# Optimization experiments

Hardware: AMD Instinct MI355X
Metric: run time of the kernel (lower is better)

## Reference

```python
import jax, jax.numpy as jnp
import numpy as np

N = 50000        # n_nodes
E = 640000       # n_edges
D = 128          # d_model (in_dim == out_dim)
H = 8            # num_heads
DH = D // H      # head dim = 16
EPS = 1e-5


def _batchnorm(x, g, b):
    # BatchNorm1d, training-mode batch statistics (biased variance)
    mu = jnp.mean(x, axis=0)
    var = jnp.mean((x - mu) ** 2, axis=0)
    return (x - mu) * jax.lax.rsqrt(var + EPS) * g + b


def setup_inputs() -> dict:
    key = jax.random.key(0)
    ks = jax.random.split(key, 16)
    s = 0.05
    h = jax.random.normal(ks[0], (N, D), jnp.float32)
    src = jax.random.randint(ks[1], (E,), 0, N)
    # guarantee every node has >= 1 incoming edge (avoids z == 0)
    dst = jnp.concatenate([jnp.arange(N), jax.random.randint(ks[2], (E - N,), 0, N)])
    return {
        "h": h,
        "src": src,
        "dst": dst,
        "WQ": jax.random.normal(ks[3], (D, D), jnp.float32) * s,
        "WK": jax.random.normal(ks[4], (D, D), jnp.float32) * s,
        "WV": jax.random.normal(ks[5], (D, D), jnp.float32) * s,
        "WO": jax.random.normal(ks[6], (D, D), jnp.float32) * s,
        "bO": jnp.zeros((D,), jnp.float32),
        "W1": jax.random.normal(ks[7], (2 * D, D), jnp.float32) * s,
        "b1": jnp.zeros((2 * D,), jnp.float32),
        "W2": jax.random.normal(ks[8], (D, 2 * D), jnp.float32) * s,
        "b2": jnp.zeros((D,), jnp.float32),
        "bn1_g": jnp.ones((D,), jnp.float32),
        "bn1_b": jnp.zeros((D,), jnp.float32),
        "bn2_g": jnp.ones((D,), jnp.float32),
        "bn2_b": jnp.zeros((D,), jnp.float32),
    }


def reference(h, src, dst, WQ, WK, WV, WO, bO, W1, b1, W2, b2, bn1_g, bn1_b, bn2_g, bn2_b):
    n = h.shape[0]
    # projections -> [N, H, DH]
    Q = (h @ WQ.T).reshape(n, H, DH)
    K = (h @ WK.T).reshape(n, H, DH)
    V = (h @ WV.T).reshape(n, H, DH)
    # per-edge score: sum(K[src] * Q[dst]) -> [E, H]; clamp/exp (scaled_exp)
    score = jnp.sum(K[src] * Q[dst], axis=-1) / np.sqrt(DH)
    score = jnp.exp(jnp.clip(score, -5.0, 5.0))
    # scatter-sum weighted values and normalizers to destination nodes
    wV = jax.ops.segment_sum(V[src] * score[..., None], dst, num_segments=n)  # [N,H,DH]
    z = jax.ops.segment_sum(score, dst, num_segments=n)                       # [N,H]
    attn = (wV / z[..., None]).reshape(n, D)
    # O projection + residual + BN1
    h1 = _batchnorm(h + (attn @ WO.T + bO), bn1_g, bn1_b)
    # FFN + residual + BN2
    f = jax.nn.relu(h1 @ W1.T + b1) @ W2.T + b2
    return _batchnorm(h1 + f, bn2_g, bn2_b)
```

## Files before the change

### kernel.cpp

```cpp
#include <hip/hip_runtime.h>
#include <math.h>


#define ND128 16384
typedef _Float16 f16;
typedef __attribute__((ext_vector_type(8))) _Float16 h8;
typedef __attribute__((ext_vector_type(4))) _Float16 h4;
typedef __attribute__((ext_vector_type(2))) _Float16 h2;
typedef __attribute__((ext_vector_type(4))) float f4;
typedef __attribute__((ext_vector_type(2))) float ff2;

__device__ __forceinline__ ff2 fp8x2_dec(unsigned v) {
#if __has_builtin(__builtin_amdgcn_cvt_pk_f32_fp8)
    return __builtin_amdgcn_cvt_pk_f32_fp8((int)v, false);
#else
    ff2 r;
    unsigned b0 = v & 0xffu, b1 = (v >> 8) & 0xffu;
    {
        unsigned e = (b0 >> 3) & 15u, m = b0 & 7u;
        float x = e ? __uint_as_float(((e + 120u) << 23) | (m << 20)) : (float)m * 0.001953125f;
        r.x = (b0 & 0x80u) ? -x : x;
    }
    {
        unsigned e = (b1 >> 3) & 15u, m = b1 & 7u;
        float x = e ? __uint_as_float(((e + 120u) << 23) | (m << 20)) : (float)m * 0.001953125f;
        r.y = (b1 & 0x80u) ? -x : x;
    }
    return r;
#endif
}

#if !__has_builtin(__builtin_amdgcn_cvt_pk_fp8_f32)
__device__ __forceinline__ unsigned char fp8_1(float f) {
    float a = fabsf(f);
    unsigned sg = (__float_as_uint(f) >> 31) << 7;
    if (a >= 448.f) return (unsigned char)(sg | 0x7E);
    if (a < 0.0009765625f) return (unsigned char)sg;
    int E; float m = frexpf(a, &E);
    if (E - 1 < -6) {
        int q = (int)rintf(a * 512.f);
        if (q > 7) return (unsigned char)(sg | 0x08);
        return (unsigned char)(sg | q);
    }
    int q = (int)rintf(m * 16.f);
    if (q == 16) { q = 8; E += 1; }
    int Ef = E - 1 + 7;
    if (Ef > 15) return (unsigned char)(sg | 0x7E);
    return (unsigned char)(sg | (Ef << 3) | (q - 8));
}
#endif

__device__ __forceinline__ unsigned fp8_pack4(float a0, float a1, float a2, float a3) {
#if __has_builtin(__builtin_amdgcn_cvt_pk_fp8_f32)
    int pk = __builtin_amdgcn_cvt_pk_fp8_f32(a0, a1, 0, false);
    pk = __builtin_amdgcn_cvt_pk_fp8_f32(a2, a3, pk, true);
    return (unsigned)pk;
#else
    return (unsigned)fp8_1(a0) | ((unsigned)fp8_1(a1) << 8) |
           ((unsigned)fp8_1(a2) << 16) | ((unsigned)fp8_1(a3) << 24);
#endif
}

__global__ __launch_bounds__(256) void k_prep(
    const float* __restrict__ h, f16* __restrict__ hb,
    const float* __restrict__ WQ, const float* __restrict__ WK,
    const float* __restrict__ WV, const float* __restrict__ WO,
    const float* __restrict__ W2,
    f16* __restrict__ Wqb, f16* __restrict__ Wkb,
    f16* __restrict__ Wvb, f16* __restrict__ Wob, f16* __restrict__ W2b,
    float* __restrict__ bn, int* __restrict__ cursor, int N)
{
    const int slab = blockIdx.x;
    const int tid = threadIdx.x;
    if (tid < 128) {
        int ci = slab * 128 + tid;
        if (ci < N) cursor[ci] = 0;
    }
    if (slab == 6) { bn[tid] = 0.f; bn[tid + 256] = 0.f; }
#pragma unroll
    for (int it = 0; it < 8; ++it) {
        int cid = it * 256 + tid;
        int lane = cid & 63;
        int m = (cid >> 6) & 7;
        int kb = cid >> 9;
        int row = slab * 128 + m * 16 + (lane & 15);
        int col = kb * 32 + (lane >> 4) * 8;
        f16 o8[8];
        if (row < N) {
            const float* p = h + (size_t)row * 128 + col;
            float4 f0 = *(const float4*)p;
            float4 f1 = *(const float4*)(p + 4);
            o8[0] = (f16)f0.x; o8[1] = (f16)f0.y; o8[2] = (f16)f0.z; o8[3] = (f16)f0.w;
            o8[4] = (f16)f1.x; o8[5] = (f16)f1.y; o8[6] = (f16)f1.z; o8[7] = (f16)f1.w;
        } else {
#pragma unroll
            for (int j = 0; j < 8; ++j) o8[j] = (f16)0.f;
        }
        *(h8*)(hb + (size_t)slab * ND128 + (size_t)cid * 8) = *(const h8*)o8;
    }
    if (slab < 6) {
        const float* Wsrc; f16* dst; int K, base;
        if (slab < 4) {
            Wsrc = slab == 0 ? WQ : slab == 1 ? WK : slab == 2 ? WV : WO;
            dst  = slab == 0 ? Wqb : slab == 1 ? Wkb : slab == 2 ? Wvb : Wob;
            K = 128; base = 0;
        } else {
            Wsrc = W2; dst = W2b; K = 256; base = (slab - 4) * 2048;
        }
#pragma unroll
        for (int it = 0; it < 8; ++it) {
            int cid = base + it * 256 + tid;
            int lane = cid & 63;
            int kb, nt;
            if (K == 128) { kb = (cid >> 6) & 3; nt = cid >> 8; }
            else          { kb = (cid >> 6) & 7; nt = cid >> 9; }
            int row = nt * 16 + (lane & 15);
            int col = kb * 32 + (lane >> 4) * 8;
            const float* p = Wsrc + (size_t)row * K + col;
            f16 o8[8];
#pragma unroll
            for (int j = 0; j < 8; ++j) o8[j] = (f16)p[j];
            *(h8*)(dst + (size_t)cid * 8) = *(const h8*)o8;
        }
    }
}

__global__ __launch_bounds__(256) void k_qkv(
    const f16* __restrict__ hb, const f16* __restrict__ Wqb,
    const f16* __restrict__ Wkb, const f16* __restrict__ Wvb,
    f16* __restrict__ Qb, unsigned char* __restrict__ Kb8,
    unsigned char* __restrict__ Vb8, int N)
{
    const int slab = blockIdx.x, oidx = blockIdx.y;
    const int w = threadIdx.x >> 6, lane = threadIdx.x & 63;
    const f16* __restrict__ Wb = oidx == 0 ? Wqb : oidx == 1 ? Wkb : Wvb;
    const f16* A = hb + (size_t)slab * ND128;

    h8 bfr[2][4];
#pragma unroll
    for (int nt = 0; nt < 2; ++nt)
#pragma unroll
        for (int kb = 0; kb < 4; ++kb)
            bfr[nt][kb] = *(const h8*)(Wb + (size_t)(((2 * w + nt) * 4 + kb) * 64 + lane) * 8);

    f4 acc[8][2];
    f4 zero = {0.f, 0.f, 0.f, 0.f};
#pragma unroll
    for (int m = 0; m < 8; ++m) { acc[m][0] = zero; acc[m][1] = zero; }

#pragma unroll
    for (int m = 0; m < 8; ++m) {
#pragma unroll
        for (int kb = 0; kb < 4; ++kb) {
            h8 a = *(const h8*)(A + (size_t)((kb * 8 + m) * 64 + lane) * 8);
            acc[m][0] = __builtin_amdgcn_mfma_f32_16x16x32_f16(bfr[0][kb], a, acc[m][0], 0, 0, 0);
            acc[m][1] = __builtin_amdgcn_mfma_f32_16x16x32_f16(bfr[1][kb], a, acc[m][1], 0, 0, 0);
        }
    }

    const int rl = lane & 15, quad = lane >> 4;
    if (oidx == 0) {
#pragma unroll
        for (int m = 0; m < 8; ++m) {
            int gr = slab * 128 + m * 16 + rl;
            if (gr < N) {
#pragma unroll
                for (int nt = 0; nt < 2; ++nt) {
                    h4 o;
                    o[0] = (f16)acc[m][nt][0]; o[1] = (f16)acc[m][nt][1];
                    o[2] = (f16)acc[m][nt][2]; o[3] = (f16)acc[m][nt][3];
                    *(h4*)(Qb + (size_t)gr * 128 + w * 32 + nt * 16 + quad * 4) = o;
                }
            }
        }
    } else {
        unsigned char* __restrict__ O8 = oidx == 1 ? Kb8 : Vb8;
#pragma unroll
        for (int m = 0; m < 8; ++m) {
            int gr = slab * 128 + m * 16 + rl;
            if (gr < N) {
#pragma unroll
                for (int nt = 0; nt < 2; ++nt) {
                    unsigned pk = fp8_pack4(acc[m][nt][0], acc[m][nt][1],
                                            acc[m][nt][2], acc[m][nt][3]);
                    *(unsigned*)(O8 + (size_t)gr * 128 + w * 32 + nt * 16 + quad * 4) = pk;
                }
            }
        }
    }
}

__global__ __launch_bounds__(256) void k_hist(
    const int* __restrict__ dst, int* __restrict__ cursor, int E)
{
    int e = blockIdx.x * 256 + threadIdx.x;
    if (e < E) atomicAdd(&cursor[dst[e]], 1);
}

__global__ __launch_bounds__(256) void k_scanA(
    const int* __restrict__ cnt, int* __restrict__ bsum, int N)
{
    const int t = threadIdx.x;
    int base = blockIdx.x * 2048 + t * 8;
    int s = 0;
#pragma unroll
    for (int j = 0; j < 8; ++j) {
        int idx = base + j;
        if (idx < N) s += cnt[idx];
    }
#pragma unroll
    for (int off = 32; off; off >>= 1) s += __shfl_down(s, off, 64);
    __shared__ int ws4[4];
    if ((t & 63) == 0) ws4[t >> 6] = s;
    __syncthreads();
    if (t == 0) bsum[blockIdx.x] = ws4[0] + ws4[1] + ws4[2] + ws4[3];
}

__global__ __launch_bounds__(256) void k_scanC(
    const int* __restrict__ cnt, const int* __restrict__ bsum,
    int* __restrict__ rowptr, int* __restrict__ cursor, int N, int nsb)
{
    const int t = threadIdx.x, b = blockIdx.x;
    __shared__ int sboff;
    if (t == 0) {
        int r = 0;
        for (int i2 = 0; i2 < b; ++i2) r += bsum[i2];
        sboff = r;
    }
    if (t == 64 && b == nsb - 1) {
        int r = 0;
        for (int i2 = 0; i2 < nsb; ++i2) r += bsum[i2];
        rowptr[N] = r;
    }
    int base = b * 2048 + t * 8;
    int loc[8];
    int s = 0;
#pragma unroll
    for (int j = 0; j < 8; ++j) {
        int idx = base + j;
        loc[j] = (idx < N) ? cnt[idx] : 0;
        s += loc[j];
    }
    __shared__ int part[256];
    part[t] = s;
    __syncthreads();
    for (int off = 1; off < 256; off <<= 1) {
        int v = (t >= off) ? part[t - off] : 0;
        __syncthreads();
        part[t] += v;
        __syncthreads();
    }
    int run = sboff + (t ? part[t - 1] : 0);
#pragma unroll
    for (int j = 0; j < 8; ++j) {
        int idx = base + j;
        if (idx < N) { rowptr[idx] = run; cursor[idx] = run; run += loc[j]; }
    }
}

__global__ __launch_bounds__(256) void k_scatter(
    const int* __restrict__ src, const int* __restrict__ dst,
    int* __restrict__ cursor, int* __restrict__ csr_src, int E)
{
    int e = blockIdx.x * 256 + threadIdx.x;
    if (e < E) {
        int pos = atomicAdd(&cursor[dst[e]], 1);
        csr_src[pos] = src[e];
    }
}

__global__ __launch_bounds__(256) void k_attn(
    const f16* __restrict__ Qb, const unsigned char* __restrict__ Kb8,
    const unsigned char* __restrict__ Vb8,
    const int* __restrict__ rowptr, const int* __restrict__ csr_src,
    f16* __restrict__ attnf, int N)
{
    const int node = blockIdx.x * 4 + (threadIdx.x >> 6);
    const int lane = threadIdx.x & 63;
    if (node >= N) return;
    const int beg = rowptr[node], end = rowptr[node + 1];
    const h2 q2 = ((const h2*)(Qb + (size_t)node * 128))[lane];
    const float qx = (float)q2[0], qy = (float)q2[1];
    float axA = 0.f, ayA = 0.f, axB = 0.f, ayB = 0.f, zA = 0.f, zB = 0.f;
    int i = beg;
    for (; i + 3 < end; i += 4) {
        int s0 = csr_src[i], s1 = csr_src[i + 1];
        int s2 = csr_src[i + 2], s3 = csr_src[i + 3];
        unsigned k0 = *(const unsigned short*)(Kb8 + (size_t)s0 * 128 + 2 * lane);
        unsigned k1 = *(const unsigned short*)(Kb8 + (size_t)s1 * 128 + 2 * lane);
        unsigned k2 = *(const unsigned short*)(Kb8 + (size_t)s2 * 128 + 2 * lane);
        unsigned k3 = *(const unsigned short*)(Kb8 + (size_t)s3 * 128 + 2 * lane);
        unsigned v0 = *(const unsigned short*)(Vb8 + (size_t)s0 * 128 + 2 * lane);
        unsigned v1 = *(const unsigned short*)(Vb8 + (size_t)s1 * 128 + 2 * lane);
        unsigned v2 = *(const unsigned short*)(Vb8 + (size_t)s2 * 128 + 2 * lane);
        unsigned v3 = *(const unsigned short*)(Vb8 + (size_t)s3 * 128 + 2 * lane);
        ff2 kf0 = fp8x2_dec(k0), kf1 = fp8x2_dec(k1);
        ff2 kf2 = fp8x2_dec(k2), kf3 = fp8x2_dec(k3);
        float p0 = fmaf(qx, kf0.x, qy * kf0.y);
        float p1 = fmaf(qx, kf1.x, qy * kf1.y);
        float p2 = fmaf(qx, kf2.x, qy * kf2.y);
        float p3 = fmaf(qx, kf3.x, qy * kf3.y);
        p0 += __shfl_xor(p0, 4, 8); p1 += __shfl_xor(p1, 4, 8);
        p2 += __shfl_xor(p2, 4, 8); p3 += __shfl_xor(p3, 4, 8);
        p0 += __shfl_xor(p0, 2, 8); p1 += __shfl_xor(p1, 2, 8);
        p2 += __shfl_xor(p2, 2, 8); p3 += __shfl_xor(p3, 2, 8);
        p0 += __shfl_xor(p0, 1, 8); p1 += __shfl_xor(p1, 1, 8);
        p2 += __shfl_xor(p2, 1, 8); p3 += __shfl_xor(p3, 1, 8);
        float sc0 = __expf(fminf(fmaxf(p0 * 0.25f, -5.f), 5.f));
        float sc1 = __expf(fminf(fmaxf(p1 * 0.25f, -5.f), 5.f));
        float sc2 = __expf(fminf(fmaxf(p2 * 0.25f, -5.f), 5.f));
        float sc3 = __expf(fminf(fmaxf(p3 * 0.25f, -5.f), 5.f));
        ff2 vf0 = fp8x2_dec(v0), vf1 = fp8x2_dec(v1);
        ff2 vf2 = fp8x2_dec(v2), vf3 = fp8x2_dec(v3);
        axA = fmaf(vf0.x, sc0, axA); ayA = fmaf(vf0.y, sc0, ayA);
        axB = fmaf(vf1.x, sc1, axB); ayB = fmaf(vf1.y, sc1, ayB);
        axA = fmaf(vf2.x, sc2, axA); ayA = fmaf(vf2.y, sc2, ayA);
        axB = fmaf(vf3.x, sc3, axB); ayB = fmaf(vf3.y, sc3, ayB);
        zA += sc0 + sc2; zB += sc1 + sc3;
    }
    for (; i < end; ++i) {
        int s0 = csr_src[i];
        unsigned k0 = *(const unsigned short*)(Kb8 + (size_t)s0 * 128 + 2 * lane);
        unsigned v0 = *(const unsigned short*)(Vb8 + (size_t)s0 * 128 + 2 * lane);
        ff2 kf0 = fp8x2_dec(k0);
        float p0 = fmaf(qx, kf0.x, qy * kf0.y);
        p0 += __shfl_xor(p0, 4, 8); p0 += __shfl_xor(p0, 2, 8); p0 += __shfl_xor(p0, 1, 8);
        float sc0 = __expf(fminf(fmaxf(p0 * 0.25f, -5.f), 5.f));
        ff2 vf0 = fp8x2_dec(v0);
        axA = fmaf(vf0.x, sc0, axA); ayA = fmaf(vf0.y, sc0, ayA);
        zA += sc0;
    }
    float inv = 1.f / (zA + zB);
    h2 o2;
    o2[0] = (f16)((axA + axB) * inv);
    o2[1] = (f16)((ayA + ayB) * inv);
    int slab = node >> 7, m = (node >> 4) & 7, lr = node & 15;
    int kb = lane >> 4, quad2 = (lane & 15) >> 2, j = (lane & 3) * 2;
    *(h2*)(attnf + (size_t)slab * ND128 +
           (size_t)(((kb * 8 + m) * 64 + lr + 16 * quad2) * 8 + j)) = o2;
}

__global__ __launch_bounds__(256) void k_oproj(
    const f16* __restrict__ attnf, const f16* __restrict__ Wob,
    const float* __restrict__ h, const float* __restrict__ bO,
    f16* __restrict__ t1b, float* __restrict__ bn, int N)
{
    __shared__ float csum[128], csq[128];
    const int tid = threadIdx.x, slab = blockIdx.x;
    const int w = tid >> 6, lane = tid & 63;
    if (tid < 128) { csum[tid] = 0.f; csq[tid] = 0.f; }
    __syncthreads();
    const f16* A = attnf + (size_t)slab * ND128;

    h8 bfr[2][4];
#pragma unroll
    for (int nt = 0; nt < 2; ++nt)
#pragma unroll
        for (int kb = 0; kb < 4; ++kb)
            bfr[nt][kb] = *(const h8*)(Wob + (size_t)(((2 * w + nt) * 4 + kb) * 64 + lane) * 8);

    f4 acc[8][2];
    f4 zero = {0.f, 0.f, 0.f, 0.f};
#pragma unroll
    for (int m = 0; m < 8; ++m) { acc[m][0] = zero; acc[m][1] = zero; }
#pragma unroll
    for (int m = 0; m < 8; ++m) {
#pragma unroll
        for (int kb = 0; kb < 4; ++kb) {
            h8 a = *(const h8*)(A + (size_t)((kb * 8 + m) * 64 + lane) * 8);
            acc[m][0] = __builtin_amdgcn_mfma_f32_16x16x32_f16(bfr[0][kb], a, acc[m][0], 0, 0, 0);
            acc[m][1] = __builtin_amdgcn_mfma_f32_16x16x32_f16(bfr[1][kb], a, acc[m][1], 0, 0, 0);
        }
    }

    const int rl = lane & 15, quad = lane >> 4;
    float4 bo[2];
#pragma unroll
    for (int nt = 0; nt < 2; ++nt)
        bo[nt] = *(const float4*)(bO + w * 32 + nt * 16 + quad * 4);
    float pcs[2][4], pcq[2][4];
#pragma unroll
    for (int nt = 0; nt < 2; ++nt)
#pragma unroll
        for (int r = 0; r < 4; ++r) { pcs[nt][r] = 0.f; pcq[nt][r] = 0.f; }

#pragma unroll
    for (int m = 0; m < 8; ++m) {
        int gr = slab * 128 + m * 16 + rl;
        if (gr < N) {
#pragma unroll
            for (int nt = 0; nt < 2; ++nt) {
                int col0 = w * 32 + nt * 16 + quad * 4;
                float4 hv = *(const float4*)(h + (size_t)gr * 128 + col0);
                float v0 = acc[m][nt][0] + hv.x + bo[nt].x;
                float v1 = acc[m][nt][1] + hv.y + bo[nt].y;
                float v2 = acc[m][nt][2] + hv.z + bo[nt].z;
                float v3 = acc[m][nt][3] + hv.w + bo[nt].w;
                h4 o; o[0] = (f16)v0; o[1] = (f16)v1; o[2] = (f16)v2; o[3] = (f16)v3;
                *(h4*)(t1b + (size_t)slab * ND128 +
                       (size_t)(((w * 8 + m) * 64 + (nt * 2 + (quad >> 1)) * 16 + rl) * 8 +
                                (quad & 1) * 4)) = o;
                pcs[nt][0] += v0; pcq[nt][0] += v0 * v0;
                pcs[nt][1] += v1; pcq[nt][1] += v1 * v1;
                pcs[nt][2] += v2; pcq[nt][2] += v2 * v2;
                pcs[nt][3] += v3; pcq[nt][3] += v3 * v3;
            }
        }
    }
#pragma unroll
    for (int nt = 0; nt < 2; ++nt)
#pragma unroll
        for (int r = 0; r < 4; ++r) {
            float s = pcs[nt][r], q = pcq[nt][r];
            s += __shfl_xor(s, 8, 16); q += __shfl_xor(q, 8, 16);
            s += __shfl_xor(s, 4, 16); q += __shfl_xor(q, 4, 16);
            s += __shfl_xor(s, 2, 16); q += __shfl_xor(q, 2, 16);
            s += __shfl_xor(s, 1, 16); q += __shfl_xor(q, 1, 16);
            if (rl == 0) {
                int cl = w * 32 + nt * 16 + quad * 4 + r;
                atomicAdd(&csum[cl], s);
                atomicAdd(&csq[cl], q);
            }
        }
    __syncthreads();
    if (tid < 128) {
        atomicAdd(bn + tid, csum[tid]);
        atomicAdd(bn + 128 + tid, csq[tid]);
    }
}

__global__ __launch_bounds__(128) void k_fold1(
    const float* __restrict__ bn, const float* __restrict__ g1,
    const float* __restrict__ bb1, const float* __restrict__ W1,
    const float* __restrict__ b1, f16* __restrict__ W1b,
    float* __restrict__ badj, float* __restrict__ sfold,
    float* __restrict__ bfold, int N)
{
    const int o = blockIdx.x, i = threadIdx.x;
    float invN = 1.f / (float)N;
    float mu = bn[i] * invN;
    float var = bn[128 + i] * invN - mu * mu;
    float s = g1[i] * rsqrtf(var + 1e-5f);
    float bb = bb1[i] - mu * s;
    if (o == 0) { sfold[i] = s; bfold[i] = bb; }
    float wv = W1[(size_t)o * 128 + i];
    __shared__ float red[128];
    red[i] = wv * bb;
    const int nt = o >> 4, lanelow = o & 15;
    const int kb = i >> 5, quad = (i >> 3) & 3, j = i & 7;
    W1b[(size_t)(((nt * 4 + kb) * 64 + lanelow + 16 * quad) * 8 + j)] = (f16)(wv * s);
    __syncthreads();
#pragma unroll
    for (int off = 64; off; off >>= 1) {
        if (i < off) red[i] += red[i + off];
        __syncthreads();
    }
    if (i == 0) badj[o] = b1[o] + red[0];
}

__global__ __launch_bounds__(256) void k_ffn1(
    const f16* __restrict__ t1b, const f16* __restrict__ W1b,
    const float* __restrict__ badj, f16* __restrict__ ub, int N)
{
    const int slab = blockIdx.x, ch = blockIdx.y;
    const int w = threadIdx.x >> 6, lane = threadIdx.x & 63;
    const f16* A = t1b + (size_t)slab * ND128;

    h8 bfr[2][4];
#pragma unroll
    for (int nt = 0; nt < 2; ++nt)
#pragma unroll
        for (int kb = 0; kb < 4; ++kb) {
            int ntg = ch * 8 + 2 * w + nt;
            bfr[nt][kb] = *(const h8*)(W1b + (size_t)((ntg * 4 + kb) * 64 + lane) * 8);
        }

    f4 acc[8][2];
    f4 zero = {0.f, 0.f, 0.f, 0.f};
#pragma unroll
    for (int m = 0; m < 8; ++m) { acc[m][0] = zero; acc[m][1] = zero; }
#pragma unroll
    for (int m = 0; m < 8; ++m) {
#pragma unroll
        for (int kb = 0; kb < 4; ++kb) {
            h8 a = *(const h8*)(A + (size_t)((kb * 8 + m) * 64 + lane) * 8);
            acc[m][0] = __builtin_amdgcn_mfma_f32_16x16x32_f16(bfr[0][kb], a, acc[m][0], 0, 0, 0);
            acc[m][1] = __builtin_amdgcn_mfma_f32_16x16x32_f16(bfr[1][kb], a, acc[m][1], 0, 0, 0);
        }
    }

    const int rl = lane & 15, quad = lane >> 4;
    const int kbu = ch * 4 + w;
    float4 ba[2];
#pragma unroll
    for (int nt = 0; nt < 2; ++nt)
        ba[nt] = *(const float4*)(badj + ch * 128 + w * 32 + nt * 16 + quad * 4);
#pragma unroll
    for (int m = 0; m < 8; ++m) {
        int gr = slab * 128 + m * 16 + rl;
        if (gr < N) {
#pragma unroll
            for (int nt = 0; nt < 2; ++nt) {
                h4 o;
                o[0] = (f16)fmaxf(acc[m][nt][0] + ba[nt].x, 0.f);
                o[1] = (f16)fmaxf(acc[m][nt][1] + ba[nt].y, 0.f);
                o[2] = (f16)fmaxf(acc[m][nt][2] + ba[nt].z, 0.f);
                o[3] = (f16)fmaxf(acc[m][nt][3] + ba[nt].w, 0.f);
                *(h4*)(ub + (size_t)slab * 32768 +
                       (size_t)(((kbu * 8 + m) * 64 + (nt * 2 + (quad >> 1)) * 16 + rl) * 8 +
                                (quad & 1) * 4)) = o;
            }
        }
    }
}

__global__ __launch_bounds__(256) void k_ffn2(
    const f16* __restrict__ ub, const f16* __restrict__ W2b,
    const f16* __restrict__ t1b,
    const float* __restrict__ sfold, const float* __restrict__ bfold,
    const float* __restrict__ b2, float* __restrict__ out,
    float* __restrict__ bn, int N)
{
    __shared__ float csum[128], csq[128], sS[128], sB[128];
    const int tid = threadIdx.x, slab = blockIdx.x;
    const int w = tid >> 6, lane = tid & 63;
    if (tid < 128) {
        csum[tid] = 0.f; csq[tid] = 0.f;
        sS[tid] = sfold[tid]; sB[tid] = bfold[tid] + b2[tid];
    }
    __syncthreads();
    const f16* A = ub + (size_t)slab * 32768;
    const f16* T1 = t1b + (size_t)slab * ND128;

    h8 bfr[2][8];
#pragma unroll
    for (int nt = 0; nt < 2; ++nt)
#pragma unroll
        for (int kb = 0; kb < 8; ++kb)
            bfr[nt][kb] = *(const h8*)(W2b + (size_t)(((2 * w + nt) * 8 + kb) * 64 + lane) * 8);

    f4 acc[8][2];
    f4 zero = {0.f, 0.f, 0.f, 0.f};
#pragma unroll
    for (int m = 0; m < 8; ++m) { acc[m][0] = zero; acc[m][1] = zero; }
#pragma unroll
    for (int m = 0; m < 8; ++m) {
#pragma unroll
        for (int kb = 0; kb < 8; ++kb) {
            h8 a = *(const h8*)(A + (size_t)((kb * 8 + m) * 64 + lane) * 8);
            acc[m][0] = __builtin_amdgcn_mfma_f32_16x16x32_f16(bfr[0][kb], a, acc[m][0], 0, 0, 0);
            acc[m][1] = __builtin_amdgcn_mfma_f32_16x16x32_f16(bfr[1][kb], a, acc[m][1], 0, 0, 0);
        }
    }

    const int rl = lane & 15, quad = lane >> 4;
    float pcs[2][4], pcq[2][4];
#pragma unroll
    for (int nt = 0; nt < 2; ++nt)
#pragma unroll
        for (int r = 0; r < 4; ++r) { pcs[nt][r] = 0.f; pcq[nt][r] = 0.f; }

#pragma unroll
    for (int m = 0; m < 8; ++m) {
        int gr = slab * 128 + m * 16 + rl;
        if (gr < N) {
#pragma unroll
            for (int nt = 0; nt < 2; ++nt) {
                int col0 = w * 32 + nt * 16 + quad * 4;
                h4 t1v = *(const h4*)(T1 +
                    (size_t)(((w * 8 + m) * 64 + (nt * 2 + (quad >> 1)) * 16 + rl) * 8 +
                             (quad & 1) * 4));
                float4 ss = *(const float4*)&sS[col0];
                float4 sb = *(const float4*)&sB[col0];
                float4 o;
                o.x = acc[m][nt][0] + fmaf(ss.x, (float)t1v[0], sb.x);
                o.y = acc[m][nt][1] + fmaf(ss.y, (float)t1v[1], sb.y);
                o.z = acc[m][nt][2] + fmaf(ss.z, (float)t1v[2], sb.z);
                o.w = acc[m][nt][3] + fmaf(ss.w, (float)t1v[3], sb.w);
                *(float4*)(out + (size_t)gr * 128 + col0) = o;
                pcs[nt][0] += o.x; pcq[nt][0] += o.x * o.x;
                pcs[nt][1] += o.y; pcq[nt][1] += o.y * o.y;
                pcs[nt][2] += o.z; pcq[nt][2] += o.z * o.z;
                pcs[nt][3] += o.w; pcq[nt][3] += o.w * o.w;
            }
        }
    }
#pragma unroll
    for (int nt = 0; nt < 2; ++nt)
#pragma unroll
        for (int r = 0; r < 4; ++r) {
            float s = pcs[nt][r], q = pcq[nt][r];
            s += __shfl_xor(s, 8, 16); q += __shfl_xor(q, 8, 16);
            s += __shfl_xor(s, 4, 16); q += __shfl_xor(q, 4, 16);
            s += __shfl_xor(s, 2, 16); q += __shfl_xor(q, 2, 16);
            s += __shfl_xor(s, 1, 16); q += __shfl_xor(q, 1, 16);
            if (rl == 0) {
                int cl = w * 32 + nt * 16 + quad * 4 + r;
                atomicAdd(&csum[cl], s);
                atomicAdd(&csq[cl], q);
            }
        }
    __syncthreads();
    if (tid < 128) {
        atomicAdd(bn + 256 + tid, csum[tid]);
        atomicAdd(bn + 384 + tid, csq[tid]);
    }
}

__global__ __launch_bounds__(256) void k_bn2(
    float* __restrict__ out, const float* __restrict__ bn,
    const float* __restrict__ g2, const float* __restrict__ bb2, int N)
{
    __shared__ float sS[128], sB[128];
    const int tid = threadIdx.x;
    if (tid < 128) {
        float invN = 1.f / (float)N;
        float mu = bn[256 + tid] * invN;
        float var = bn[384 + tid] * invN - mu * mu;
        float scl = g2[tid] * rsqrtf(var + 1e-5f);
        sS[tid] = scl;
        sB[tid] = bb2[tid] - mu * scl;
    }
    __syncthreads();
    size_t idx = (size_t)blockIdx.x * 256 + tid;
    size_t total = (size_t)N * 32;
    if (idx < total) {
        int c0 = (int)((idx * 4) & 127);
        float4 v = *(const float4*)(out + idx * 4);
        v.x = fmaf(v.x, sS[c0 + 0], sB[c0 + 0]);
        v.y = fmaf(v.y, sS[c0 + 1], sB[c0 + 1]);
        v.z = fmaf(v.z, sS[c0 + 2], sB[c0 + 2]);
        v.w = fmaf(v.w, sS[c0 + 3], sB[c0 + 3]);
        *(float4*)(out + idx * 4) = v;
    }
}

extern "C" void kernel_launch(void* const* d_in, const int* in_sizes, int n_in,
                              void* d_out, int out_size, void* d_ws, size_t ws_size,
                              hipStream_t stream)
{
    const float* h   = (const float*)d_in[0];
    const int*   src = (const int*)d_in[1];
    const int*   dst = (const int*)d_in[2];
    const float* WQ  = (const float*)d_in[3];
    const float* WK  = (const float*)d_in[4];
    const float* WV  = (const float*)d_in[5];
    const float* WO  = (const float*)d_in[6];
    const float* bO  = (const float*)d_in[7];
    const float* W1  = (const float*)d_in[8];
    const float* b1  = (const float*)d_in[9];
    const float* W2  = (const float*)d_in[10];
    const float* b2  = (const float*)d_in[11];
    const float* g1  = (const float*)d_in[12];
    const float* bb1 = (const float*)d_in[13];
    const float* g2  = (const float*)d_in[14];
    const float* bb2 = (const float*)d_in[15];
    float* out = (float*)d_out;

    int N = in_sizes[0] / 128;
    int E = in_sizes[1];
    const int slabs = (N + 127) / 128;
    const int nsb = (N + 2047) / 2048;
    const size_t B1 = (size_t)slabs * 32768;

    char* Wp = (char*)d_ws;
    f16* hb  = (f16*)Wp;
    f16* Qb  = (f16*)(Wp + B1);
    unsigned char* Kb8 = (unsigned char*)(Wp + 2 * B1);
    unsigned char* Vb8 = (unsigned char*)(Wp + 2 * B1 + B1 / 2);
    f16* ub  = (f16*)(Wp + B1);
    f16* t1b = (f16*)(Wp + 3 * B1);
    const size_t base = 4 * B1;
    f16* Wqb = (f16*)(Wp + base);
    f16* Wkb = (f16*)(Wp + base + 32768);
    f16* Wvb = (f16*)(Wp + base + 65536);
    f16* Wob = (f16*)(Wp + base + 98304);
    f16* W1b = (f16*)(Wp + base + 131072);
    f16* W2b = (f16*)(Wp + base + 196608);
    float* badj  = (float*)(Wp + base + 262144);
    float* sfold = (float*)(Wp + base + 263168);
    float* bfold = (float*)(Wp + base + 263680);
    float* bn    = (float*)(Wp + base + 264192);
    int* cursor  = (int*)(Wp + base + 266240);
    int* rowptr  = (int*)(Wp + base + 266240 + (size_t)N * 4);
    int* csr     = (int*)(Wp + base + 266240 + (size_t)N * 8 + 8);
    int* bsum    = (int*)((char*)csr + (size_t)E * 4);

    k_prep<<<slabs, 256, 0, stream>>>(h, hb, WQ, WK, WV, WO, W2,
                                      Wqb, Wkb, Wvb, Wob, W2b, bn, cursor, N);
    k_qkv<<<dim3(slabs, 3), 256, 0, stream>>>(hb, Wqb, Wkb, Wvb, Qb, Kb8, Vb8, N);
    k_hist<<<(E + 255) / 256, 256, 0, stream>>>(dst, cursor, E);
    k_scanA<<<nsb, 256, 0, stream>>>(cursor, bsum, N);
    k_scanC<<<nsb, 256, 0, stream>>>(cursor, bsum, rowptr, cursor, N, nsb);
    k_scatter<<<(E + 255) / 256, 256, 0, stream>>>(src, dst, cursor, csr, E);
    k_attn<<<(N + 3) / 4, 256, 0, stream>>>(Qb, Kb8, Vb8, rowptr, csr, hb, N);
    k_oproj<<<slabs, 256, 0, stream>>>(hb, Wob, h, bO, t1b, bn, N);
    k_fold1<<<256, 128, 0, stream>>>(bn, g1, bb1, W1, b1, W1b, badj, sfold, bfold, N);
    k_ffn1<<<dim3(slabs, 2), 256, 0, stream>>>(t1b, W1b, badj, ub, N);
    k_ffn2<<<slabs, 256, 0, stream>>>(ub, W2b, t1b, sfold, bfold, b2, out, bn, N);
    k_bn2<<<(int)(((size_t)N * 32 + 255) / 256), 256, 0, stream>>>(out, bn, g2, bb2, N);
}
```

Measured before the change: 318.6 us.

## Process 8 edges per wave in attention and split GEMM slabs across twice as many blocks

The attention kernel is restructured so each wave handles 8 edges at once. Each lane owns one head and loads a full 16-byte K/V chunk, and partial sums are combined across edge groups with shuffles at the end. This replaces the old scheme of one edge per step with 2-byte loads per lane, aiming for wider memory transactions and more independent gathers in flight. Separately, the prep, QKV, O-projection and FFN kernels split each 128-row slab into two half-slab blocks to raise block count and occupancy, at the cost of reloading weight fragments twice and doubling the BN-stat atomics.

```diff
diff --git a/kernel.cpp b/kernel.cpp
--- a/kernel.cpp
+++ b/kernel.cpp
@@ -27,6 +27,21 @@
         r.y = (b1 & 0x80u) ? -x : x;
     }
     return r;
+#endif
+}
+
+__device__ __forceinline__ ff2 dec_lo(unsigned v) {
+#if __has_builtin(__builtin_amdgcn_cvt_pk_f32_fp8)
+    return __builtin_amdgcn_cvt_pk_f32_fp8((int)v, false);
+#else
+    return fp8x2_dec(v & 0xffffu);
+#endif
+}
+__device__ __forceinline__ ff2 dec_hi(unsigned v) {
+#if __has_builtin(__builtin_amdgcn_cvt_pk_f32_fp8)
+    return __builtin_amdgcn_cvt_pk_f32_fp8((int)v, true);
+#else
+    return fp8x2_dec((v >> 16) & 0xffffu);
 #endif
 }
 
@@ -70,15 +85,18 @@
     f16* __restrict__ Wvb, f16* __restrict__ Wob, f16* __restrict__ W2b,
     float* __restrict__ bn, int* __restrict__ cursor, int N)
 {
-    const int slab = blockIdx.x;
+    const int slab = blockIdx.x, my = blockIdx.y;
     const int tid = threadIdx.x;
-    if (tid < 128) {
-        int ci = slab * 128 + tid;
-        if (ci < N) cursor[ci] = 0;
-    }
-    if (slab == 6) { bn[tid] = 0.f; bn[tid + 256] = 0.f; }
-#pragma unroll
-    for (int it = 0; it < 8; ++it) {
+    if (my == 0) {
+        if (tid < 128) {
+            int ci = slab * 128 + tid;
+            if (ci < N) cursor[ci] = 0;
+        }
+        if (slab == 6) { bn[tid] = 0.f; bn[tid + 256] = 0.f; }
+    }
+#pragma unroll
+    for (int it2 = 0; it2 < 4; ++it2) {
+        int it = my * 4 + it2;
         int cid = it * 256 + tid;
         int lane = cid & 63;
         int m = (cid >> 6) & 7;
@@ -98,7 +116,7 @@
         }
         *(h8*)(hb + (size_t)slab * ND128 + (size_t)cid * 8) = *(const h8*)o8;
     }
-    if (slab < 6) {
+    if (slab < 6 && my == 1) {
         const float* Wsrc; f16* dst; int K, base;
         if (slab < 4) {
             Wsrc = slab == 0 ? WQ : slab == 1 ? WK : slab == 2 ? WV : WO;
@@ -131,7 +149,7 @@
     f16* __restrict__ Qb, unsigned char* __restrict__ Kb8,
     unsigned char* __restrict__ Vb8, int N)
 {
-    const int slab = blockIdx.x, oidx = blockIdx.y;
+    const int slab = blockIdx.x, oidx = blockIdx.y, mh = blockIdx.z;
     const int w = threadIdx.x >> 6, lane = threadIdx.x & 63;
     const f16* __restrict__ Wb = oidx == 0 ? Wqb : oidx == 1 ? Wkb : Wvb;
     const f16* A = hb + (size_t)slab * ND128;
@@ -143,16 +161,17 @@
         for (int kb = 0; kb < 4; ++kb)
             bfr[nt][kb] = *(const h8*)(Wb + (size_t)(((2 * w + nt) * 4 + kb) * 64 + lane) * 8);
 
-    f4 acc[8][2];
+    f4 acc[4][2];
     f4 zero = {0.f, 0.f, 0.f, 0.f};
 #pragma unroll
-    for (int m = 0; m < 8; ++m) { acc[m][0] = zero; acc[m][1] = zero; }
-
-#pragma unroll
-    for (int m = 0; m < 8; ++m) {
+    for (int m = 0; m < 4; ++m) { acc[m][0] = zero; acc[m][1] = zero; }
+
+#pragma unroll
+    for (int m = 0; m < 4; ++m) {
+        int mg = mh * 4 + m;
 #pragma unroll
         for (int kb = 0; kb < 4; ++kb) {
-            h8 a = *(const h8*)(A + (size_t)((kb * 8 + m) * 64 + lane) * 8);
+            h8 a = *(const h8*)(A + (size_t)((kb * 8 + mg) * 64 + lane) * 8);
             acc[m][0] = __builtin_amdgcn_mfma_f32_16x16x32_f16(bfr[0][kb], a, acc[m][0], 0, 0, 0);
             acc[m][1] = __builtin_amdgcn_mfma_f32_16x16x32_f16(bfr[1][kb], a, acc[m][1], 0, 0, 0);
         }
@@ -161,8 +180,8 @@
     const int rl = lane & 15, quad = lane >> 4;
     if (oidx == 0) {
 #pragma unroll
-        for (int m = 0; m < 8; ++m) {
-            int gr = slab * 128 + m * 16 + rl;
+        for (int m = 0; m < 4; ++m) {
+            int gr = slab * 128 + (mh * 4 + m) * 16 + rl;
             if (gr < N) {
 #pragma unroll
                 for (int nt = 0; nt < 2; ++nt) {
@@ -176,8 +195,8 @@
     } else {
         unsigned char* __restrict__ O8 = oidx == 1 ? Kb8 : Vb8;
 #pragma unroll
-        for (int m = 0; m < 8; ++m) {
-            int gr = slab * 128 + m * 16 + rl;
+        for (int m = 0; m < 4; ++m) {
+            int gr = slab * 128 + (mh * 4 + m) * 16 + rl;
             if (gr < N) {
 #pragma unroll
                 for (int nt = 0; nt < 2; ++nt) {
@@ -278,66 +297,79 @@
     const int node = blockIdx.x * 4 + (threadIdx.x >> 6);
     const int lane = threadIdx.x & 63;
     if (node >= N) return;
+    const int e = lane >> 3;
+    const int hd = lane & 7;
     const int beg = rowptr[node], end = rowptr[node + 1];
-    const h2 q2 = ((const h2*)(Qb + (size_t)node * 128))[lane];
-    const float qx = (float)q2[0], qy = (float)q2[1];
-    float axA = 0.f, ayA = 0.f, axB = 0.f, ayB = 0.f, zA = 0.f, zB = 0.f;
-    int i = beg;
-    for (; i + 3 < end; i += 4) {
-        int s0 = csr_src[i], s1 = csr_src[i + 1];
-        int s2 = csr_src[i + 2], s3 = csr_src[i + 3];
-        unsigned k0 = *(const unsigned short*)(Kb8 + (size_t)s0 * 128 + 2 * lane);
-        unsigned k1 = *(const unsigned short*)(Kb8 + (size_t)s1 * 128 + 2 * lane);
-        unsigned k2 = *(const unsigned short*)(Kb8 + (size_t)s2 * 128 + 2 * lane);
-        unsigned k3 = *(const unsigned short*)(Kb8 + (size_t)s3 * 128 + 2 * lane);
-        unsigned v0 = *(const unsigned short*)(Vb8 + (size_t)s0 * 128 + 2 * lane);
-        unsigned v1 = *(const unsigned short*)(Vb8 + (size_t)s1 * 128 + 2 * lane);
-        unsigned v2 = *(const unsigned short*)(Vb8 + (size_t)s2 * 128 + 2 * lane);
-        unsigned v3 = *(const unsigned short*)(Vb8 + (size_t)s3 * 128 + 2 * lane);
-        ff2 kf0 = fp8x2_dec(k0), kf1 = fp8x2_dec(k1);
-        ff2 kf2 = fp8x2_dec(k2), kf3 = fp8x2_dec(k3);
-        float p0 = fmaf(qx, kf0.x, qy * kf0.y);
-        float p1 = fmaf(qx, kf1.x, qy * kf1.y);
-        float p2 = fmaf(qx, kf2.x, qy * kf2.y);
-        float p3 = fmaf(qx, kf3.x, qy * kf3.y);
-        p0 += __shfl_xor(p0, 4, 8); p1 += __shfl_xor(p1, 4, 8);
-        p2 += __shfl_xor(p2, 4, 8); p3 += __shfl_xor(p3, 4, 8);
-        p0 += __shfl_xor(p0, 2, 8); p1 += __shfl_xor(p1, 2, 8);
-        p2 += __shfl_xor(p2, 2, 8); p3 += __shfl_xor(p3, 2, 8);
-        p0 += __shfl_xor(p0, 1, 8); p1 += __shfl_xor(p1, 1, 8);
-        p2 += __shfl_xor(p2, 1, 8); p3 += __shfl_xor(p3, 1, 8);
-        float sc0 = __expf(fminf(fmaxf(p0 * 0.25f, -5.f), 5.f));
-        float sc1 = __expf(fminf(fmaxf(p1 * 0.25f, -5.f), 5.f));
-        float sc2 = __expf(fminf(fmaxf(p2 * 0.25f, -5.f), 5.f));
-        float sc3 = __expf(fminf(fmaxf(p3 * 0.25f, -5.f), 5.f));
-        ff2 vf0 = fp8x2_dec(v0), vf1 = fp8x2_dec(v1);
-        ff2 vf2 = fp8x2_dec(v2), vf3 = fp8x2_dec(v3);
-        axA = fmaf(vf0.x, sc0, axA); ayA = fmaf(vf0.y, sc0, ayA);
-        axB = fmaf(vf1.x, sc1, axB); ayB = fmaf(vf1.y, sc1, ayB);
-        axA = fmaf(vf2.x, sc2, axA); ayA = fmaf(vf2.y, sc2, ayA);
-        axB = fmaf(vf3.x, sc3, axB); ayB = fmaf(vf3.y, sc3, ayB);
-        zA += sc0 + sc2; zB += sc1 + sc3;
-    }
-    for (; i < end; ++i) {
-        int s0 = csr_src[i];
-        unsigned k0 = *(const unsigned short*)(Kb8 + (size_t)s0 * 128 + 2 * lane);
-        unsigned v0 = *(const unsigned short*)(Vb8 + (size_t)s0 * 128 + 2 * lane);
-        ff2 kf0 = fp8x2_dec(k0);
-        float p0 = fmaf(qx, kf0.x, qy * kf0.y);
-        p0 += __shfl_xor(p0, 4, 8); p0 += __shfl_xor(p0, 2, 8); p0 += __shfl_xor(p0, 1, 8);
-        float sc0 = __expf(fminf(fmaxf(p0 * 0.25f, -5.f), 5.f));
-        ff2 vf0 = fp8x2_dec(v0);
-        axA = fmaf(vf0.x, sc0, axA); ayA = fmaf(vf0.y, sc0, ayA);
-        zA += sc0;
-    }
-    float inv = 1.f / (zA + zB);
-    h2 o2;
-    o2[0] = (f16)((axA + axB) * inv);
-    o2[1] = (f16)((ayA + ayB) * inv);
-    int slab = node >> 7, m = (node >> 4) & 7, lr = node & 15;
-    int kb = lane >> 4, quad2 = (lane & 15) >> 2, j = (lane & 3) * 2;
-    *(h2*)(attnf + (size_t)slab * ND128 +
-           (size_t)(((kb * 8 + m) * 64 + lr + 16 * quad2) * 8 + j)) = o2;
+
+    float q[16];
+    {
+        const h8* qp = (const h8*)(Qb + (size_t)node * 128 + hd * 16);
+        h8 q0 = qp[0], q1 = qp[1];
+#pragma unroll
+        for (int j = 0; j < 8; ++j) { q[j] = (float)q0[j]; q[8 + j] = (float)q1[j]; }
+    }
+
+    float acc[16];
+#pragma unroll
+    for (int c = 0; c < 16; ++c) acc[c] = 0.f;
+    float z = 0.f;
+
+    for (int i = beg; i < end; i += 8) {
+        int eidx = i + e;
+        bool valid = eidx < end;
+        int s = csr_src[valid ? eidx : end - 1];
+        const uint4 kv = *(const uint4*)(Kb8 + (size_t)s * 128 + hd * 16);
+        const uint4 vv = *(const uint4*)(Vb8 + (size_t)s * 128 + hd * 16);
+
+        ff2 k0 = dec_lo(kv.x), k1 = dec_hi(kv.x), k2 = dec_lo(kv.y), k3 = dec_hi(kv.y);
+        ff2 k4 = dec_lo(kv.z), k5 = dec_hi(kv.z), k6 = dec_lo(kv.w), k7 = dec_hi(kv.w);
+        float pa = q[0] * k0.x, pb = q[1] * k0.y;
+        pa = fmaf(q[2],  k1.x, pa); pb = fmaf(q[3],  k1.y, pb);
+        pa = fmaf(q[4],  k2.x, pa); pb = fmaf(q[5],  k2.y, pb);
+        pa = fmaf(q[6],  k3.x, pa); pb = fmaf(q[7],  k3.y, pb);
+        pa = fmaf(q[8],  k4.x, pa); pb = fmaf(q[9],  k4.y, pb);
+        pa = fmaf(q[10], k5.x, pa); pb = fmaf(q[11], k5.y, pb);
+        pa = fmaf(q[12], k6.x, pa); pb = fmaf(q[13], k6.y, pb);
+        pa = fmaf(q[14], k7.x, pa); pb = fmaf(q[15], k7.y, pb);
+        float p = pa + pb;
+
+        float sc = __expf(fminf(fmaxf(p * 0.25f, -5.f), 5.f));
+        sc = valid ? sc : 0.f;
+        z += sc;
+
+        ff2 v0 = dec_lo(vv.x), v1 = dec_hi(vv.x), v2 = dec_lo(vv.y), v3 = dec_hi(vv.y);
+        ff2 v4 = dec_lo(vv.z), v5 = dec_hi(vv.z), v6 = dec_lo(vv.w), v7 = dec_hi(vv.w);
+        acc[0]  = fmaf(v0.x, sc, acc[0]);  acc[1]  = fmaf(v0.y, sc, acc[1]);
+        acc[2]  = fmaf(v1.x, sc, acc[2]);  acc[3]  = fmaf(v1.y, sc, acc[3]);
+        acc[4]  = fmaf(v2.x, sc, acc[4]);  acc[5]  = fmaf(v2.y, sc, acc[5]);
+        acc[6]  = fmaf(v3.x, sc, acc[6]);  acc[7]  = fmaf(v3.y, sc, acc[7]);
+        acc[8]  = fmaf(v4.x, sc, acc[8]);  acc[9]  = fmaf(v4.y, sc, acc[9]);
+        acc[10] = fmaf(v5.x, sc, acc[10]); acc[11] = fmaf(v5.y, sc, acc[11]);
+        acc[12] = fmaf(v6.x, sc, acc[12]); acc[13] = fmaf(v6.y, sc, acc[13]);
+        acc[14] = fmaf(v7.x, sc, acc[14]); acc[15] = fmaf(v7.y, sc, acc[15]);
+    }
+
+#pragma unroll
+    for (int c = 0; c < 16; ++c) {
+        acc[c] += __shfl_xor(acc[c], 8, 64);
+        acc[c] += __shfl_xor(acc[c], 16, 64);
+        acc[c] += __shfl_xor(acc[c], 32, 64);
+    }
+    z += __shfl_xor(z, 8, 64);
+    z += __shfl_xor(z, 16, 64);
+    z += __shfl_xor(z, 32, 64);
+    float inv = 1.f / z;
+
+    if (e < 2) {
+        h8 o;
+#pragma unroll
+        for (int j = 0; j < 8; ++j) o[j] = (f16)(acc[e * 8 + j] * inv);
+        int slab = node >> 7, m = (node >> 4) & 7, lr = node & 15;
+        int kb = hd >> 1;
+        int quad2 = (hd & 1) * 2 + e;
+        *(h8*)(attnf + (size_t)slab * ND128 +
+               (size_t)(((kb * 8 + m) * 64 + lr + 16 * quad2) * 8)) = o;
+    }
 }
 
 __global__ __launch_bounds__(256) void k_oproj(
@@ -346,7 +378,7 @@
     f16* __restrict__ t1b, float* __restrict__ bn, int N)
 {
     __shared__ float csum[128], csq[128];
-    const int tid = threadIdx.x, slab = blockIdx.x;
+    const int tid = threadIdx.x, slab = blockIdx.x, mh = blockIdx.y;
     const int w = tid >> 6, lane = tid & 63;
     if (tid < 128) { csum[tid] = 0.f; csq[tid] = 0.f; }
     __syncthreads();
@@ -359,15 +391,16 @@
         for (int kb = 0; kb < 4; ++kb)
             bfr[nt][kb] = *(const h8*)(Wob + (size_t)(((2 * w + nt) * 4 + kb) * 64 + lane) * 8);
 
-    f4 acc[8][2];
+    f4 acc[4][2];
     f4 zero = {0.f, 0.f, 0.f, 0.f};
 #pragma unroll
-    for (int m = 0; m < 8; ++m) { acc[m][0] = zero; acc[m][1] = zero; }
-#pragma unroll
-    for (int m = 0; m < 8; ++m) {
+    for (int m = 0; m < 4; ++m) { acc[m][0] = zero; acc[m][1] = zero; }
+#pragma unroll
+    for (int m = 0; m < 4; ++m) {
+        int mg = mh * 4 + m;
 #pragma unroll
         for (int kb = 0; kb < 4; ++kb) {
-            h8 a = *(const h8*)(A + (size_t)((kb * 8 + m) * 64 + lane) * 8);
+            h8 a = *(const h8*)(A + (size_t)((kb * 8 + mg) * 64 + lane) * 8);
             acc[m][0] = __builtin_amdgcn_mfma_f32_16x16x32_f16(bfr[0][kb], a, acc[m][0], 0, 0, 0);
             acc[m][1] = __builtin_amdgcn_mfma_f32_16x16x32_f16(bfr[1][kb], a, acc[m][1], 0, 0, 0);
         }
@@ -385,8 +418,9 @@
         for (int r = 0; r < 4; ++r) { pcs[nt][r] = 0.f; pcq[nt][r] = 0.f; }
 
 #pragma unroll
-    for (int m = 0; m < 8; ++m) {
-        int gr = slab * 128 + m * 16 + rl;
+    for (int m = 0; m < 4; ++m) {
+        int mg = mh * 4 + m;
+        int gr = slab * 128 + mg * 16 + rl;
         if (gr < N) {
 #pragma unroll
             for (int nt = 0; nt < 2; ++nt) {
@@ -398,7 +432,7 @@
                 float v3 = acc[m][nt][3] + hv.w + bo[nt].w;
                 h4 o; o[0] = (f16)v0; o[1] = (f16)v1; o[2] = (f16)v2; o[3] = (f16)v3;
                 *(h4*)(t1b + (size_t)slab * ND128 +
-                       (size_t)(((w * 8 + m) * 64 + (nt * 2 + (quad >> 1)) * 16 + rl) * 8 +
+                       (size_t)(((w * 8 + mg) * 64 + (nt * 2 + (quad >> 1)) * 16 + rl) * 8 +
                                 (quad & 1) * 4)) = o;
                 pcs[nt][0] += v0; pcq[nt][0] += v0 * v0;
                 pcs[nt][1] += v1; pcq[nt][1] += v1 * v1;
@@ -462,7 +496,7 @@
     const f16* __restrict__ t1b, const f16* __restrict__ W1b,
     const float* __restrict__ badj, f16* __restrict__ ub, int N)
 {
-    const int slab = blockIdx.x, ch = blockIdx.y;
+    const int slab = blockIdx.x, ch = blockIdx.y, mh = blockIdx.z;
     const int w = threadIdx.x >> 6, lane = threadIdx.x & 63;
     const f16* A = t1b + (size_t)slab * ND128;
 
@@ -475,15 +509,16 @@
             bfr[nt][kb] = *(const h8*)(W1b + (size_t)((ntg * 4 + kb) * 64 + lane) * 8);
         }
 
-    f4 acc[8][2];
+    f4 acc[4][2];
     f4 zero = {0.f, 0.f, 0.f, 0.f};
 #pragma unroll
-    for (int m = 0; m < 8; ++m) { acc[m][0] = zero; acc[m][1] = zero; }
-#pragma unroll
-    for (int m = 0; m < 8; ++m) {
+    for (int m = 0; m < 4; ++m) { acc[m][0] = zero; acc[m][1] = zero; }
+#pragma unroll
+    for (int m = 0; m < 4; ++m) {
+        int mg = mh * 4 + m;
 #pragma unroll
         for (int kb = 0; kb < 4; ++kb) {
-            h8 a = *(const h8*)(A + (size_t)((kb * 8 + m) * 64 + lane) * 8);
+            h8 a = *(const h8*)(A + (size_t)((kb * 8 + mg) * 64 + lane) * 8);
             acc[m][0] = __builtin_amdgcn_mfma_f32_16x16x32_f16(bfr[0][kb], a, acc[m][0], 0, 0, 0);
             acc[m][1] = __builtin_amdgcn_mfma_f32_16x16x32_f16(bfr[1][kb], a, acc[m][1], 0, 0, 0);
         }
@@ -496,8 +531,9 @@
     for (int nt = 0; nt < 2; ++nt)
         ba[nt] = *(const float4*)(badj + ch * 128 + w * 32 + nt * 16 + quad * 4);
 #pragma unroll
-    for (int m = 0; m < 8; ++m) {
-        int gr = slab * 128 + m * 16 + rl;
+    for (int m = 0; m < 4; ++m) {
+        int mg = mh * 4 + m;
+        int gr = slab * 128 + mg * 16 + rl;
         if (gr < N) {
 #pragma unroll
             for (int nt = 0; nt < 2; ++nt) {
@@ -507,7 +543,7 @@
                 o[2] = (f16)fmaxf(acc[m][nt][2] + ba[nt].z, 0.f);
                 o[3] = (f16)fmaxf(acc[m][nt][3] + ba[nt].w, 0.f);
                 *(h4*)(ub + (size_t)slab * 32768 +
-                       (size_t)(((kbu * 8 + m) * 64 + (nt * 2 + (quad >> 1)) * 16 + rl) * 8 +
+                       (size_t)(((kbu * 8 + mg) * 64 + (nt * 2 + (quad >> 1)) * 16 + rl) * 8 +
                                 (quad & 1) * 4)) = o;
             }
         }
@@ -522,7 +558,7 @@
     float* __restrict__ bn, int N)
 {
     __shared__ float csum[128], csq[128], sS[128], sB[128];
-    const int tid = threadIdx.x, slab = blockIdx.x;
+    const int tid = threadIdx.x, slab = blockIdx.x, mh = blockIdx.y;
     const int w = tid >> 6, lane = tid & 63;
     if (tid < 128) {
         csum[tid] = 0.f; csq[tid] = 0.f;
@@ -539,15 +575,16 @@
         for (int kb = 0; kb < 8; ++kb)
             bfr[nt][kb] = *(const h8*)(W2b + (size_t)(((2 * w + nt) * 8 + kb) * 64 + lane) * 8);
 
-    f4 acc[8][2];
+    f4 acc[4][2];
     f4 zero = {0.f, 0.f, 0.f, 0.f};
 #pragma unroll
-    for (int m = 0; m < 8; ++m) { acc[m][0] = zero; acc[m][1] = zero; }
-#pragma unroll
-    for (int m = 0; m < 8; ++m) {
+    for (int m = 0; m < 4; ++m) { acc[m][0] = zero; acc[m][1] = zero; }
+#pragma unroll
+    for (int m = 0; m < 4; ++m) {
+        int mg = mh * 4 + m;
 #pragma unroll
         for (int kb = 0; kb < 8; ++kb) {
-            h8 a = *(const h8*)(A + (size_t)((kb * 8 + m) * 64 + lane) * 8);
+            h8 a = *(const h8*)(A + (size_t)((kb * 8 + mg) * 64 + lane) * 8);
             acc[m][0] = __builtin_amdgcn_mfma_f32_16x16x32_f16(bfr[0][kb], a, acc[m][0], 0, 0, 0);
             acc[m][1] = __builtin_amdgcn_mfma_f32_16x16x32_f16(bfr[1][kb], a, acc[m][1], 0, 0, 0);
         }
@@ -561,14 +598,15 @@
         for (int r = 0; r < 4; ++r) { pcs[nt][r] = 0.f; pcq[nt][r] = 0.f; }
 
 #pragma unroll
-    for (int m = 0; m < 8; ++m) {
-        int gr = slab * 128 + m * 16 + rl;
+    for (int m = 0; m < 4; ++m) {
+        int mg = mh * 4 + m;
+        int gr = slab * 128 + mg * 16 + rl;
         if (gr < N) {
 #pragma unroll
             for (int nt = 0; nt < 2; ++nt) {
                 int col0 = w * 32 + nt * 16 + quad * 4;
                 h4 t1v = *(const h4*)(T1 +
-                    (size_t)(((w * 8 + m) * 64 + (nt * 2 + (quad >> 1)) * 16 + rl) * 8 +
+                    (size_t)(((w * 8 + mg) * 64 + (nt * 2 + (quad >> 1)) * 16 + rl) * 8 +
                              (quad & 1) * 4));
                 float4 ss = *(const float4*)&sS[col0];
                 float4 sb = *(const float4*)&sB[col0];
@@ -686,17 +724,17 @@
     int* csr     = (int*)(Wp + base + 266240 + (size_t)N * 8 + 8);
     int* bsum    = (int*)((char*)csr + (size_t)E * 4);
 
-    k_prep<<<slabs, 256, 0, stream>>>(h, hb, WQ, WK, WV, WO, W2,
-                                      Wqb, Wkb, Wvb, Wob, W2b, bn, cursor, N);
-    k_qkv<<<dim3(slabs, 3), 256, 0, stream>>>(hb, Wqb, Wkb, Wvb, Qb, Kb8, Vb8, N);
+    k_prep<<<dim3(slabs, 2), 256, 0, stream>>>(h, hb, WQ, WK, WV, WO, W2,
+                                               Wqb, Wkb, Wvb, Wob, W2b, bn, cursor, N);
+    k_qkv<<<dim3(slabs, 3, 2), 256, 0, stream>>>(hb, Wqb, Wkb, Wvb, Qb, Kb8, Vb8, N);
     k_hist<<<(E + 255) / 256, 256, 0, stream>>>(dst, cursor, E);
     k_scanA<<<nsb, 256, 0, stream>>>(cursor, bsum, N);
     k_scanC<<<nsb, 256, 0, stream>>>(cursor, bsum, rowptr, cursor, N, nsb);
     k_scatter<<<(E + 255) / 256, 256, 0, stream>>>(src, dst, cursor, csr, E);
     k_attn<<<(N + 3) / 4, 256, 0, stream>>>(Qb, Kb8, Vb8, rowptr, csr, hb, N);
-    k_oproj<<<slabs, 256, 0, stream>>>(hb, Wob, h, bO, t1b, bn, N);
+    k_oproj<<<dim3(slabs, 2), 256, 0, stream>>>(hb, Wob, h, bO, t1b, bn, N);
     k_fold1<<<256, 128, 0, stream>>>(bn, g1, bb1, W1, b1, W1b, badj, sfold, bfold, N);
-    k_ffn1<<<dim3(slabs, 2), 256, 0, stream>>>(t1b, W1b, badj, ub, N);
-    k_ffn2<<<slabs, 256, 0, stream>>>(ub, W2b, t1b, sfold, bfold, b2, out, bn, N);
+    k_ffn1<<<dim3(slabs, 2, 2), 256, 0, stream>>>(t1b, W1b, badj, ub, N);
+    k_ffn2<<<dim3(slabs, 2), 256, 0, stream>>>(ub, W2b, t1b, sfold, bfold, b2, out, bn, N);
     k_bn2<<<(int)(((size_t)N * 32 + 255) / 256), 256, 0, stream>>>(out, bn, g2, bb2, N);
 }
```

New measurement: 327.4 us. 2.8% more time.
